# Optimization experiments

Hardware: AMD Instinct MI355X
Metric: run time of the kernel (lower is better)

## Reference

```python
import jax, jax.numpy as jnp
import numpy as np

EMBED = 512
HEADS = 8
DIM_HEAD = 64
SCALE = DIM_HEAD ** -0.5


def setup_inputs() -> dict:
    key = jax.random.key(0)
    k1, k2, k3 = jax.random.split(key, 3)
    x = jax.random.normal(k1, (1, EMBED, 64, 64), dtype=jnp.float32)
    # nn.Linear(embed, 3*embed) weight [out, in] -> store transposed [in, out] for x @ W
    W_qkv = jax.random.normal(k2, (EMBED, 3 * EMBED), dtype=jnp.float32) * (EMBED ** -0.5)
    b_qkv = jax.random.normal(k3, (3 * EMBED,), dtype=jnp.float32) * 0.01
    return {"x": x, "W_qkv": W_qkv, "b_qkv": b_qkv}


def reference(x, W_qkv, b_qkv):
    B, E, h, w = x.shape
    N = h * w
    # [B, E, H, W] -> [B, N, E]
    xs = x.reshape(B, E, N).transpose(0, 2, 1)
    qkv = xs @ W_qkv + b_qkv                      # [B, N, 3E]
    q, k, v = jnp.split(qkv, 3, axis=-1)          # each [B, N, E]

    def heads(t):
        return t.reshape(B, N, HEADS, DIM_HEAD).transpose(0, 2, 1, 3)  # [B, H, N, dh]

    q, k, v = heads(q), heads(k), heads(v)
    # raw (non-softmax) attention scores, materialized as in the original
    attn = jnp.einsum('bhqd,bhkd->bhqk', q, k) * SCALE  # [B, H, N, N]
    coarse_attn = attn.sum(axis=-2)                     # sum over queries -> [B, H, N]
    output = jnp.einsum('bhqk,bhkd->bhqd', attn, v)     # [B, H, N, dh]
    return coarse_attn, output
```

## Files before the change

### kernel.cpp

```cpp
#include <hip/hip_runtime.h>


#define N_TOK 4096
#define EMBED 512
#define J3    1536
#define HEADS 8
#define DH    64
#define SCALE 0.125f

typedef float  floatx4  __attribute__((ext_vector_type(4)));
typedef short  shortx8  __attribute__((ext_vector_type(8)));
typedef unsigned short ushortx4 __attribute__((ext_vector_type(4)));
typedef unsigned int u32;
typedef unsigned short ushort;

__device__ inline ushort f2bf(float f) {
    union { float f; u32 u; } x; x.f = f;
    u32 r = x.u + 0x7fffu + ((x.u >> 16) & 1u);
    return (ushort)(r >> 16);
}
__device__ inline float bf2f(ushort u) {
    union { u32 u; float f; } x; x.u = ((u32)u) << 16; return x.f;
}
__device__ static inline void async_copy16(void* lds, const void* g) {
    auto* gp = (const __attribute__((address_space(1))) u32*)g;
    auto* lp = (__attribute__((address_space(3))) u32*)lds;
    __builtin_amdgcn_global_load_lds(gp, lp, 16, 0, 0);
}
__device__ inline int permj(int j) {
    if (j < 512) return j;
    if (j < 1024) return 512 + ((j - 512) >> 6) * 128 + ((j - 512) & 63);
    return 512 + ((j - 1024) >> 6) * 128 + 64 + ((j - 1024) & 63);
}

__global__ __launch_bounds__(256) void prep(const float* __restrict__ x,
                                            const float* __restrict__ W,
                                            ushort* __restrict__ xT,
                                            ushort* __restrict__ WT,
                                            float* __restrict__ xsum) {
    const int t = threadIdx.x;
    int bx = blockIdx.x;
    const bool isx = bx < 64;
    const float* src = isx ? x : W;
    const int C = isx ? N_TOK : J3;
    if (!isx) bx -= 64;
    __shared__ float T[64][65];
    __shared__ float red[256];
    const int c0 = bx * 64, r0 = blockIdx.y * 64;
    #pragma unroll
    for (int k = 0; k < 16; ++k) {
        int i = t + 256 * k; int r = i >> 6, c = i & 63;
        T[r][c] = src[(size_t)(r0 + r) * C + c0 + c];
    }
    __syncthreads();
    if (isx) {
        int row = t >> 2, seg = (t & 3) * 16;
        float s = 0.f;
        #pragma unroll
        for (int cc = 0; cc < 16; ++cc) s += T[row][seg + cc];
        red[t] = s;
    }
    #pragma unroll
    for (int k = 0; k < 4; ++k) {
        int i = t + 256 * k; int cr = i >> 4, cc4 = (i & 15) * 4;
        ushortx4 o = { f2bf(T[cc4 + 0][cr]), f2bf(T[cc4 + 1][cr]),
                       f2bf(T[cc4 + 2][cr]), f2bf(T[cc4 + 3][cr]) };
        int dr = isx ? (c0 + cr) : permj(c0 + cr);
        ushort* dst = isx ? xT : WT;
        *(ushortx4*)&dst[(size_t)dr * 512 + r0 + cc4] = o;
    }
    if (isx) {
        __syncthreads();
        if ((t & 3) == 0)
            atomicAdd(&xsum[r0 + (t >> 2)], red[t] + red[t + 1] + red[t + 2] + red[t + 3]);
    }
}

__global__ __launch_bounds__(256) void qkv_m(const ushort* __restrict__ xT,
                                             const ushort* __restrict__ WT,
                                             const float* __restrict__ bias,
                                             ushort* __restrict__ qkv,
                                             float* __restrict__ Mp) {
    const int bx = blockIdx.x, ch = blockIdx.y;
    const int j0 = bx * 128, n0 = ch * 128;
    const bool iskv = bx >= 4;
    const int h = bx - 4;
    __shared__ __align__(16) char lds[34816];
    short* As = (short*)lds;
    short* Bs = (short*)(lds + 8192);
    short* Kt = (short*)lds;
    short* Vt = (short*)(lds + 17408);
    const int t = threadIdx.x, lane = t & 63, w = t >> 6;
    const int wm = w & 1, wn = w >> 1;
    const int quad = lane >> 4, mrow = lane & 15;
    floatx4 acc[4][4] = {};
    for (int e0 = 0; e0 < 512; e0 += 32) {
        __syncthreads();
        #pragma unroll
        for (int s = 0; s < 2; ++s) {
            int i = t + 256 * s; int row = i >> 2, q = i & 3;
            async_copy16((char*)As + (size_t)w * 1024 + (size_t)s * 4096,
                         xT + (size_t)(n0 + row) * 512 + e0 + q * 8);
            async_copy16((char*)Bs + (size_t)w * 1024 + (size_t)s * 4096,
                         WT + (size_t)(j0 + row) * 512 + e0 + q * 8);
        }
        __syncthreads();
        shortx8 a[4], b[4];
        #pragma unroll
        for (int mi = 0; mi < 4; ++mi)
            a[mi] = *(const shortx8*)&As[(wm * 64 + mi * 16 + mrow) * 32 + quad * 8];
        #pragma unroll
        for (int ni = 0; ni < 4; ++ni)
            b[ni] = *(const shortx8*)&Bs[(wn * 64 + ni * 16 + mrow) * 32 + quad * 8];
        #pragma unroll
        for (int mi = 0; mi < 4; ++mi)
            #pragma unroll
            for (int ni = 0; ni < 4; ++ni)
                acc[mi][ni] = __builtin_amdgcn_mfma_f32_16x16x32_bf16(a[mi], b[ni], acc[mi][ni], 0, 0, 0);
    }
    __syncthreads();
    {
        short* ldst = (wn == 0) ? Kt : Vt;
        #pragma unroll
        for (int ni = 0; ni < 4; ++ni) {
            int cl = wn * 64 + ni * 16 + mrow;
            float bj;
            if (!iskv) bj = bias[j0 + cl];
            else bj = (cl < 64) ? bias[512 + h * 64 + cl] : bias[1024 + h * 64 + cl - 64];
            int dh = ni * 16 + mrow;
            #pragma unroll
            for (int mi = 0; mi < 4; ++mi)
                #pragma unroll
                for (int r = 0; r < 4; ++r) {
                    int tok = wm * 64 + mi * 16 + quad * 4 + r;
                    float v = acc[mi][ni][r] + bj;
                    ushort bf = f2bf(v);
                    if (!iskv) {
                        qkv[(size_t)(n0 + tok) * J3 + j0 + cl] = bf;
                    } else {
                        ldst[dh * 136 + tok] = (short)bf;
                        if (cl < 64)
                            qkv[(size_t)(n0 + tok) * J3 + 512 + h * 128 + cl] = bf;
                    }
                }
        }
    }
    if (!iskv) return;
    __syncthreads();
    const int dpb = (w & 1) * 32, db = (w >> 1) * 32;
    floatx4 m[2][2] = {};
    #pragma unroll
    for (int kt = 0; kt < 4; ++kt) {
        shortx8 ka[2], vb[2];
        #pragma unroll
        for (int fi = 0; fi < 2; ++fi)
            ka[fi] = *(const shortx8*)&Kt[(dpb + fi * 16 + mrow) * 136 + kt * 32 + quad * 8];
        #pragma unroll
        for (int fj = 0; fj < 2; ++fj)
            vb[fj] = *(const shortx8*)&Vt[(db + fj * 16 + mrow) * 136 + kt * 32 + quad * 8];
        #pragma unroll
        for (int fi = 0; fi < 2; ++fi)
            #pragma unroll
            for (int fj = 0; fj < 2; ++fj)
                m[fi][fj] = __builtin_amdgcn_mfma_f32_16x16x32_bf16(ka[fi], vb[fj], m[fi][fj], 0, 0, 0);
    }
    float* mp = Mp + ((size_t)h * 32 + ch) * 4096;
    #pragma unroll
    for (int fi = 0; fi < 2; ++fi)
        #pragma unroll
        for (int fj = 0; fj < 2; ++fj)
            #pragma unroll
            for (int r = 0; r < 4; ++r)
                mp[(dpb + fi * 16 + quad * 4 + r) * 64 + db + fj * 16 + mrow] = m[fi][fj][r];
}

__global__ __launch_bounds__(256) void reduce_qm(const float* __restrict__ Mp,
                                                 const ushort* __restrict__ WT,
                                                 const float* __restrict__ bias,
                                                 const float* __restrict__ xsum,
                                                 ushort* __restrict__ Mt,
                                                 float* __restrict__ qsum) {
    const int h = blockIdx.x, part = blockIdx.y;
    const int t = threadIdx.x;
    __shared__ float Msh[16][68];
    __shared__ float red[256];
    const int i0 = part * 1024 + t * 4;
    floatx4 s = {0.f, 0.f, 0.f, 0.f};
    #pragma unroll 4
    for (int c = 0; c < 32; ++c)
        s += *(const floatx4*)&Mp[((size_t)h * 32 + c) * 4096 + i0];
    const int dpl = t >> 4, d0 = (t & 15) * 4;
    *(floatx4*)&Msh[dpl][d0] = s;
    __syncthreads();
    {
        int d = t >> 2, dpl0 = (t & 3) * 4;
        ushortx4 o = { f2bf(Msh[dpl0 + 0][d]), f2bf(Msh[dpl0 + 1][d]),
                       f2bf(Msh[dpl0 + 2][d]), f2bf(Msh[dpl0 + 3][d]) };
        *(ushortx4*)&Mt[(size_t)h * 4096 + d * 64 + part * 16 + dpl0] = o;
    }
    {
        int row = t >> 4, seg = (t & 15) * 32;
        int j = h * 64 + part * 16 + row;
        float qa = 0.f;
        #pragma unroll
        for (int g = 0; g < 4; ++g) {
            shortx8 wv = *(const shortx8*)(WT + (size_t)j * 512 + seg + g * 8);
            #pragma unroll
            for (int u = 0; u < 8; ++u)
                qa += bf2f((ushort)wv[u]) * xsum[seg + g * 8 + u];
        }
        red[t] = qa;
    }
    __syncthreads();
    if (t < 16) {
        float tot = 0.f;
        #pragma unroll
        for (int g = 0; g < 16; ++g) tot += red[t * 16 + g];
        int j = h * 64 + part * 16 + t;
        qsum[j] = 4096.f * bias[j] + tot;
    }
}

__global__ __launch_bounds__(64) void out_kernel(const ushort* __restrict__ qkv,
                                                 const ushort* __restrict__ Mt,
                                                 const float* __restrict__ qsum,
                                                 float* __restrict__ out) {
    const int h = blockIdx.x, n0 = blockIdx.y * 64;
    const int lane = threadIdx.x;
    const int quad = lane >> 4, mrow = lane & 15;
    floatx4 acc[4][4] = {};
    #pragma unroll
    for (int ks = 0; ks < 2; ++ks) {
        shortx8 a[4], b[4];
        #pragma unroll
        for (int mi = 0; mi < 4; ++mi)
            a[mi] = *(const shortx8*)(qkv + (size_t)(n0 + mi * 16 + mrow) * J3 + h * DH + ks * 32 + quad * 8);
        #pragma unroll
        for (int ni = 0; ni < 4; ++ni)
            b[ni] = *(const shortx8*)(Mt + (size_t)h * 4096 + (ni * 16 + mrow) * 64 + ks * 32 + quad * 8);
        #pragma unroll
        for (int mi = 0; mi < 4; ++mi)
            #pragma unroll
            for (int ni = 0; ni < 4; ++ni)
                acc[mi][ni] = __builtin_amdgcn_mfma_f32_16x16x32_bf16(a[mi], b[ni], acc[mi][ni], 0, 0, 0);
    }
    float* op = out + HEADS * N_TOK + (size_t)h * N_TOK * DH;
    #pragma unroll
    for (int mi = 0; mi < 4; ++mi)
        #pragma unroll
        for (int r = 0; r < 4; ++r) {
            int n = n0 + mi * 16 + quad * 4 + r;
            #pragma unroll
            for (int ni = 0; ni < 4; ++ni)
                op[(size_t)n * DH + ni * 16 + mrow] = acc[mi][ni][r] * SCALE;
        }
    float ca = 0.f;
    #pragma unroll
    for (int g = 0; g < 8; ++g) {
        shortx8 kk = *(const shortx8*)(qkv + (size_t)(n0 + lane) * J3 + 512 + h * 128 + g * 8);
        #pragma unroll
        for (int j = 0; j < 8; ++j)
            ca += bf2f((ushort)kk[j]) * qsum[h * DH + g * 8 + j];
    }
    out[h * N_TOK + n0 + lane] = ca * SCALE;
}

extern "C" void kernel_launch(void* const* d_in, const int* in_sizes, int n_in,
                              void* d_out, int out_size, void* d_ws, size_t ws_size,
                              hipStream_t stream) {
    const float* x = (const float*)d_in[0];
    const float* W = (const float*)d_in[1];
    const float* b = (const float*)d_in[2];
    float* out = (float*)d_out;

    ushort* xT = (ushort*)d_ws;
    ushort* WT = xT + (size_t)N_TOK * EMBED;
    ushort* qkvb = WT + (size_t)J3 * EMBED;
    ushort* Mt = qkvb + (size_t)N_TOK * J3;
    float* Mp   = (float*)(Mt + (size_t)HEADS * DH * DH);
    float* xsum = Mp + (size_t)HEADS * 32 * 4096;
    float* qsum = xsum + 512;

    prep<<<dim3(88, 8), 256, 0, stream>>>(x, W, xT, WT, xsum);
    qkv_m<<<dim3(12, 32), 256, 0, stream>>>(xT, WT, b, qkvb, Mp);
    reduce_qm<<<dim3(8, 4), 256, 0, stream>>>(Mp, WT, b, xsum, Mt, qsum);
    out_kernel<<<dim3(8, 64), 64, 0, stream>>>(qkvb, Mt, qsum, out);
}
```

Baseline: 99.91 us.

## Fuse QKV GEMM, M reduction and output into one persistent kernel with grid barriers

```diff
diff --git a/kernel.cpp b/kernel.cpp
--- a/kernel.cpp
+++ b/kernel.cpp
@@ -31,6 +31,14 @@
     if (j < 512) return j;
     if (j < 1024) return 512 + ((j - 512) >> 6) * 128 + ((j - 512) & 63);
     return 512 + ((j - 1024) >> 6) * 128 + 64 + ((j - 1024) & 63);
+}
+__device__ inline void bar_add(int* p) {
+    __hip_atomic_fetch_add(p, 1, __ATOMIC_ACQ_REL, __HIP_MEMORY_SCOPE_AGENT);
+}
+__device__ inline void bar_spin(int* p, int tgt) {
+    while (__hip_atomic_load(p, __ATOMIC_RELAXED, __HIP_MEMORY_SCOPE_AGENT) < tgt)
+        __builtin_amdgcn_s_sleep(8);
+    (void)__hip_atomic_load(p, __ATOMIC_ACQUIRE, __HIP_MEMORY_SCOPE_AGENT);
 }
 
 __global__ __launch_bounds__(256) void prep(const float* __restrict__ x,
@@ -76,11 +84,15 @@
     }
 }
 
-__global__ __launch_bounds__(256) void qkv_m(const ushort* __restrict__ xT,
-                                             const ushort* __restrict__ WT,
-                                             const float* __restrict__ bias,
-                                             ushort* __restrict__ qkv,
-                                             float* __restrict__ Mp) {
+__global__ __launch_bounds__(256, 2) void mega(const ushort* __restrict__ xT,
+                                               const ushort* __restrict__ WT,
+                                               const float* __restrict__ bias,
+                                               const float* __restrict__ xsum,
+                                               ushort* __restrict__ Mt,
+                                               float* __restrict__ Mp,
+                                               float* __restrict__ qsum,
+                                               int* __restrict__ bars,
+                                               float* __restrict__ out) {
     const int bx = blockIdx.x, ch = blockIdx.y;
     const int j0 = bx * 128, n0 = ch * 128;
     const bool iskv = bx >= 4;
@@ -90,9 +102,13 @@
     short* Bs = (short*)(lds + 8192);
     short* Kt = (short*)lds;
     short* Vt = (short*)(lds + 17408);
+    short* Qt = (short*)lds;
+    __shared__ float Msh[16][68];
+    __shared__ float red[256];
     const int t = threadIdx.x, lane = t & 63, w = t >> 6;
     const int wm = w & 1, wn = w >> 1;
     const int quad = lane >> 4, mrow = lane & 15;
+
     floatx4 acc[4][4] = {};
     for (int e0 = 0; e0 < 512; e0 += 32) {
         __syncthreads();
@@ -119,150 +135,151 @@
                 acc[mi][ni] = __builtin_amdgcn_mfma_f32_16x16x32_bf16(a[mi], b[ni], acc[mi][ni], 0, 0, 0);
     }
     __syncthreads();
-    {
-        short* ldst = (wn == 0) ? Kt : Vt;
+
+    if (!iskv) {
         #pragma unroll
         for (int ni = 0; ni < 4; ++ni) {
             int cl = wn * 64 + ni * 16 + mrow;
-            float bj;
-            if (!iskv) bj = bias[j0 + cl];
-            else bj = (cl < 64) ? bias[512 + h * 64 + cl] : bias[1024 + h * 64 + cl - 64];
-            int dh = ni * 16 + mrow;
+            float bj = bias[j0 + cl];
             #pragma unroll
             for (int mi = 0; mi < 4; ++mi)
                 #pragma unroll
                 for (int r = 0; r < 4; ++r) {
                     int tok = wm * 64 + mi * 16 + quad * 4 + r;
-                    float v = acc[mi][ni][r] + bj;
-                    ushort bf = f2bf(v);
-                    if (!iskv) {
-                        qkv[(size_t)(n0 + tok) * J3 + j0 + cl] = bf;
-                    } else {
-                        ldst[dh * 136 + tok] = (short)bf;
-                        if (cl < 64)
-                            qkv[(size_t)(n0 + tok) * J3 + 512 + h * 128 + cl] = bf;
-                    }
+                    Qt[tok * 136 + cl] = (short)f2bf(acc[mi][ni][r] + bj);
                 }
         }
-    }
-    if (!iskv) return;
+    } else {
+        short* ldst = (wn == 0) ? Kt : Vt;
+        const int boff = (wn == 0) ? 512 : 1024;
+        #pragma unroll
+        for (int ni = 0; ni < 4; ++ni) {
+            int dh = ni * 16 + mrow;
+            float bj = bias[boff + h * 64 + dh];
+            #pragma unroll
+            for (int mi = 0; mi < 4; ++mi)
+                #pragma unroll
+                for (int r = 0; r < 4; ++r) {
+                    int tok = wm * 64 + mi * 16 + quad * 4 + r;
+                    ldst[dh * 136 + tok] = (short)f2bf(acc[mi][ni][r] + bj);
+                }
+        }
+    }
     __syncthreads();
-    const int dpb = (w & 1) * 32, db = (w >> 1) * 32;
-    floatx4 m[2][2] = {};
-    #pragma unroll
-    for (int kt = 0; kt < 4; ++kt) {
-        shortx8 ka[2], vb[2];
+
+    if (iskv) {
+        const int dpb = (w & 1) * 32, db = (w >> 1) * 32;
+        floatx4 m[2][2] = {};
+        #pragma unroll
+        for (int kt = 0; kt < 4; ++kt) {
+            shortx8 ka[2], vb[2];
+            #pragma unroll
+            for (int fi = 0; fi < 2; ++fi)
+                ka[fi] = *(const shortx8*)&Kt[(dpb + fi * 16 + mrow) * 136 + kt * 32 + quad * 8];
+            #pragma unroll
+            for (int fj = 0; fj < 2; ++fj)
+                vb[fj] = *(const shortx8*)&Vt[(db + fj * 16 + mrow) * 136 + kt * 32 + quad * 8];
+            #pragma unroll
+            for (int fi = 0; fi < 2; ++fi)
+                #pragma unroll
+                for (int fj = 0; fj < 2; ++fj)
+                    m[fi][fj] = __builtin_amdgcn_mfma_f32_16x16x32_bf16(ka[fi], vb[fj], m[fi][fj], 0, 0, 0);
+        }
+        float* mp = Mp + ((size_t)h * 32 + ch) * 4096;
         #pragma unroll
         for (int fi = 0; fi < 2; ++fi)
-            ka[fi] = *(const shortx8*)&Kt[(dpb + fi * 16 + mrow) * 136 + kt * 32 + quad * 8];
-        #pragma unroll
-        for (int fj = 0; fj < 2; ++fj)
-            vb[fj] = *(const shortx8*)&Vt[(db + fj * 16 + mrow) * 136 + kt * 32 + quad * 8];
-        #pragma unroll
-        for (int fi = 0; fi < 2; ++fi)
             #pragma unroll
             for (int fj = 0; fj < 2; ++fj)
-                m[fi][fj] = __builtin_amdgcn_mfma_f32_16x16x32_bf16(ka[fi], vb[fj], m[fi][fj], 0, 0, 0);
-    }
-    float* mp = Mp + ((size_t)h * 32 + ch) * 4096;
-    #pragma unroll
-    for (int fi = 0; fi < 2; ++fi)
-        #pragma unroll
-        for (int fj = 0; fj < 2; ++fj)
-            #pragma unroll
-            for (int r = 0; r < 4; ++r)
-                mp[(dpb + fi * 16 + quad * 4 + r) * 64 + db + fj * 16 + mrow] = m[fi][fj][r];
-}
-
-__global__ __launch_bounds__(256) void reduce_qm(const float* __restrict__ Mp,
-                                                 const ushort* __restrict__ WT,
-                                                 const float* __restrict__ bias,
-                                                 const float* __restrict__ xsum,
-                                                 ushort* __restrict__ Mt,
-                                                 float* __restrict__ qsum) {
-    const int h = blockIdx.x, part = blockIdx.y;
-    const int t = threadIdx.x;
-    __shared__ float Msh[16][68];
-    __shared__ float red[256];
-    const int i0 = part * 1024 + t * 4;
-    floatx4 s = {0.f, 0.f, 0.f, 0.f};
-    #pragma unroll 4
-    for (int c = 0; c < 32; ++c)
-        s += *(const floatx4*)&Mp[((size_t)h * 32 + c) * 4096 + i0];
-    const int dpl = t >> 4, d0 = (t & 15) * 4;
-    *(floatx4*)&Msh[dpl][d0] = s;
-    __syncthreads();
-    {
-        int d = t >> 2, dpl0 = (t & 3) * 4;
-        ushortx4 o = { f2bf(Msh[dpl0 + 0][d]), f2bf(Msh[dpl0 + 1][d]),
-                       f2bf(Msh[dpl0 + 2][d]), f2bf(Msh[dpl0 + 3][d]) };
-        *(ushortx4*)&Mt[(size_t)h * 4096 + d * 64 + part * 16 + dpl0] = o;
-    }
-    {
-        int row = t >> 4, seg = (t & 15) * 32;
-        int j = h * 64 + part * 16 + row;
-        float qa = 0.f;
-        #pragma unroll
-        for (int g = 0; g < 4; ++g) {
-            shortx8 wv = *(const shortx8*)(WT + (size_t)j * 512 + seg + g * 8);
-            #pragma unroll
-            for (int u = 0; u < 8; ++u)
-                qa += bf2f((ushort)wv[u]) * xsum[seg + g * 8 + u];
-        }
-        red[t] = qa;
-    }
-    __syncthreads();
-    if (t < 16) {
-        float tot = 0.f;
-        #pragma unroll
-        for (int g = 0; g < 16; ++g) tot += red[t * 16 + g];
-        int j = h * 64 + part * 16 + t;
-        qsum[j] = 4096.f * bias[j] + tot;
-    }
-}
-
-__global__ __launch_bounds__(64) void out_kernel(const ushort* __restrict__ qkv,
-                                                 const ushort* __restrict__ Mt,
-                                                 const float* __restrict__ qsum,
-                                                 float* __restrict__ out) {
-    const int h = blockIdx.x, n0 = blockIdx.y * 64;
-    const int lane = threadIdx.x;
-    const int quad = lane >> 4, mrow = lane & 15;
-    floatx4 acc[4][4] = {};
-    #pragma unroll
-    for (int ks = 0; ks < 2; ++ks) {
-        shortx8 a[4], b[4];
+                #pragma unroll
+                for (int r = 0; r < 4; ++r)
+                    mp[(dpb + fi * 16 + quad * 4 + r) * 64 + db + fj * 16 + mrow] = m[fi][fj][r];
+        __syncthreads();
+        if (t == 0) bar_add(&bars[0]);
+
+        if (ch < 4) {
+            if (t == 0) bar_spin(&bars[0], 256);
+            __syncthreads();
+            const int part = ch;
+            const int i0 = part * 1024 + t * 4;
+            floatx4 s = {0.f, 0.f, 0.f, 0.f};
+            #pragma unroll 4
+            for (int c = 0; c < 32; ++c)
+                s += *(const floatx4*)&Mp[((size_t)h * 32 + c) * 4096 + i0];
+            *(floatx4*)&Msh[t >> 4][(t & 15) * 4] = s;
+            {
+                int row = t >> 4, seg = (t & 15) * 32;
+                int j = h * 64 + part * 16 + row;
+                float qa = 0.f;
+                #pragma unroll
+                for (int g = 0; g < 4; ++g) {
+                    shortx8 wv = *(const shortx8*)(WT + (size_t)j * 512 + seg + g * 8);
+                    #pragma unroll
+                    for (int u = 0; u < 8; ++u)
+                        qa += bf2f((ushort)wv[u]) * xsum[seg + g * 8 + u];
+                }
+                red[t] = qa;
+            }
+            __syncthreads();
+            {
+                int d = t >> 2, dpl0 = (t & 3) * 4;
+                ushortx4 o = { f2bf(Msh[dpl0 + 0][d]), f2bf(Msh[dpl0 + 1][d]),
+                               f2bf(Msh[dpl0 + 2][d]), f2bf(Msh[dpl0 + 3][d]) };
+                *(ushortx4*)&Mt[(size_t)h * 4096 + d * 64 + part * 16 + dpl0] = o;
+            }
+            if (t < 16) {
+                float tot = 0.f;
+                #pragma unroll
+                for (int g = 0; g < 16; ++g) tot += red[t * 16 + g];
+                int j = h * 64 + part * 16 + t;
+                qsum[j] = 4096.f * bias[j] + tot;
+            }
+            __syncthreads();
+            if (t == 0) bar_add(&bars[1]);
+        }
+        if (t == 0) bar_spin(&bars[1], 32);
+        __syncthreads();
+        {
+            int tok = t >> 1, half = (t & 1) * 32;
+            float ca = 0.f;
+            #pragma unroll 8
+            for (int dp = half; dp < half + 32; ++dp)
+                ca += bf2f((ushort)Kt[dp * 136 + tok]) * qsum[h * 64 + dp];
+            red[t] = ca;
+        }
+        __syncthreads();
+        if (t < 128)
+            out[h * N_TOK + n0 + t] = (red[2 * t] + red[2 * t + 1]) * SCALE;
+    } else {
+        if (t == 0) bar_spin(&bars[1], 32);
+        __syncthreads();
+        const int h2 = 2 * bx + wn;
+        floatx4 a2[4][4] = {};
+        #pragma unroll
+        for (int ks = 0; ks < 2; ++ks) {
+            shortx8 a[4], b[4];
+            #pragma unroll
+            for (int mi = 0; mi < 4; ++mi)
+                a[mi] = *(const shortx8*)&Qt[(wm * 64 + mi * 16 + mrow) * 136 + wn * 64 + ks * 32 + quad * 8];
+            #pragma unroll
+            for (int ni = 0; ni < 4; ++ni)
+                b[ni] = *(const shortx8*)(Mt + (size_t)h2 * 4096 + (ni * 16 + mrow) * 64 + ks * 32 + quad * 8);
+            #pragma unroll
+            for (int mi = 0; mi < 4; ++mi)
+                #pragma unroll
+                for (int ni = 0; ni < 4; ++ni)
+                    a2[mi][ni] = __builtin_amdgcn_mfma_f32_16x16x32_bf16(a[mi], b[ni], a2[mi][ni], 0, 0, 0);
+        }
+        float* op = out + HEADS * N_TOK + (size_t)h2 * N_TOK * DH;
         #pragma unroll
         for (int mi = 0; mi < 4; ++mi)
-            a[mi] = *(const shortx8*)(qkv + (size_t)(n0 + mi * 16 + mrow) * J3 + h * DH + ks * 32 + quad * 8);
-        #pragma unroll
-        for (int ni = 0; ni < 4; ++ni)
-            b[ni] = *(const shortx8*)(Mt + (size_t)h * 4096 + (ni * 16 + mrow) * 64 + ks * 32 + quad * 8);
-        #pragma unroll
-        for (int mi = 0; mi < 4; ++mi)
-            #pragma unroll
-            for (int ni = 0; ni < 4; ++ni)
-                acc[mi][ni] = __builtin_amdgcn_mfma_f32_16x16x32_bf16(a[mi], b[ni], acc[mi][ni], 0, 0, 0);
-    }
-    float* op = out + HEADS * N_TOK + (size_t)h * N_TOK * DH;
-    #pragma unroll
-    for (int mi = 0; mi < 4; ++mi)
-        #pragma unroll
-        for (int r = 0; r < 4; ++r) {
-            int n = n0 + mi * 16 + quad * 4 + r;
-            #pragma unroll
-            for (int ni = 0; ni < 4; ++ni)
-                op[(size_t)n * DH + ni * 16 + mrow] = acc[mi][ni][r] * SCALE;
-        }
-    float ca = 0.f;
-    #pragma unroll
-    for (int g = 0; g < 8; ++g) {
-        shortx8 kk = *(const shortx8*)(qkv + (size_t)(n0 + lane) * J3 + 512 + h * 128 + g * 8);
-        #pragma unroll
-        for (int j = 0; j < 8; ++j)
-            ca += bf2f((ushort)kk[j]) * qsum[h * DH + g * 8 + j];
-    }
-    out[h * N_TOK + n0 + lane] = ca * SCALE;
+            #pragma unroll
+            for (int r = 0; r < 4; ++r) {
+                int n = n0 + wm * 64 + mi * 16 + quad * 4 + r;
+                #pragma unroll
+                for (int ni = 0; ni < 4; ++ni)
+                    op[(size_t)n * DH + ni * 16 + mrow] = a2[mi][ni][r] * SCALE;
+            }
+    }
 }
 
 extern "C" void kernel_launch(void* const* d_in, const int* in_sizes, int n_in,
@@ -275,14 +292,13 @@
 
     ushort* xT = (ushort*)d_ws;
     ushort* WT = xT + (size_t)N_TOK * EMBED;
-    ushort* qkvb = WT + (size_t)J3 * EMBED;
-    ushort* Mt = qkvb + (size_t)N_TOK * J3;
+    ushort* Mt = WT + (size_t)J3 * EMBED;
     float* Mp   = (float*)(Mt + (size_t)HEADS * DH * DH);
     float* xsum = Mp + (size_t)HEADS * 32 * 4096;
     float* qsum = xsum + 512;
-
+    int*   bars = (int*)(qsum + 512);
+
+    hipMemsetAsync(bars, 0, 2 * sizeof(int), stream);
     prep<<<dim3(88, 8), 256, 0, stream>>>(x, W, xT, WT, xsum);
-    qkv_m<<<dim3(12, 32), 256, 0, stream>>>(xT, WT, b, qkvb, Mp);
-    reduce_qm<<<dim3(8, 4), 256, 0, stream>>>(Mp, WT, b, xsum, Mt, qsum);
-    out_kernel<<<dim3(8, 64), 64, 0, stream>>>(qkvb, Mt, qsum, out);
-}
+    mega<<<dim3(12, 32), 256, 0, stream>>>(xT, WT, b, xsum, Mt, Mp, qsum, bars, out);
+}
```

Measured after the change: 123.4 us. 23.6% more time.

## Fuse coarse-attention into QKV kernel, halve token tile, drop K copy to global

Applied to the files above, without the earlier changes.

```diff
diff --git a/kernel.cpp b/kernel.cpp
--- a/kernel.cpp
+++ b/kernel.cpp
@@ -79,92 +79,143 @@
 __global__ __launch_bounds__(256) void qkv_m(const ushort* __restrict__ xT,
                                              const ushort* __restrict__ WT,
                                              const float* __restrict__ bias,
-                                             ushort* __restrict__ qkv,
-                                             float* __restrict__ Mp) {
+                                             const float* __restrict__ xsum,
+                                             ushort* __restrict__ Qb,
+                                             float* __restrict__ Mp,
+                                             float* __restrict__ out) {
     const int bx = blockIdx.x, ch = blockIdx.y;
-    const int j0 = bx * 128, n0 = ch * 128;
+    const int j0 = bx * 128, n0 = ch * 64;
     const bool iskv = bx >= 4;
     const int h = bx - 4;
-    __shared__ __align__(16) char lds[34816];
+    __shared__ __align__(16) char lds[18432];
     short* As = (short*)lds;
-    short* Bs = (short*)(lds + 8192);
+    short* Bs = (short*)(lds + 4096);
     short* Kt = (short*)lds;
-    short* Vt = (short*)(lds + 17408);
+    short* Vt = (short*)(lds + 9216);
+    short* Qt = (short*)lds;
+    __shared__ float cred[64 * 33];
+    __shared__ float qs[64];
     const int t = threadIdx.x, lane = t & 63, w = t >> 6;
-    const int wm = w & 1, wn = w >> 1;
     const int quad = lane >> 4, mrow = lane & 15;
-    floatx4 acc[4][4] = {};
+
+    if (iskv) {
+        int jl = t >> 2, seg = (t & 3) * 128;
+        const ushort* wr = WT + (size_t)(h * 64 + jl) * 512 + seg;
+        float qa = 0.f;
+        #pragma unroll
+        for (int g = 0; g < 16; ++g) {
+            shortx8 wv = *(const shortx8*)(wr + g * 8);
+            #pragma unroll
+            for (int u = 0; u < 8; ++u)
+                qa += bf2f((ushort)wv[u]) * xsum[seg + g * 8 + u];
+        }
+        cred[t] = qa;
+        __syncthreads();
+        if (t < 64)
+            qs[t] = 4096.f * bias[h * 64 + t]
+                  + cred[4 * t] + cred[4 * t + 1] + cred[4 * t + 2] + cred[4 * t + 3];
+    }
+
+    floatx4 acc[4][2] = {};
     for (int e0 = 0; e0 < 512; e0 += 32) {
         __syncthreads();
+        {
+            int row = t >> 2, q = t & 3;
+            async_copy16((char*)As + (size_t)w * 1024,
+                         xT + (size_t)(n0 + row) * 512 + e0 + q * 8);
+        }
         #pragma unroll
         for (int s = 0; s < 2; ++s) {
             int i = t + 256 * s; int row = i >> 2, q = i & 3;
-            async_copy16((char*)As + (size_t)w * 1024 + (size_t)s * 4096,
-                         xT + (size_t)(n0 + row) * 512 + e0 + q * 8);
             async_copy16((char*)Bs + (size_t)w * 1024 + (size_t)s * 4096,
                          WT + (size_t)(j0 + row) * 512 + e0 + q * 8);
         }
         __syncthreads();
-        shortx8 a[4], b[4];
+        shortx8 a[4], b[2];
         #pragma unroll
         for (int mi = 0; mi < 4; ++mi)
-            a[mi] = *(const shortx8*)&As[(wm * 64 + mi * 16 + mrow) * 32 + quad * 8];
-        #pragma unroll
-        for (int ni = 0; ni < 4; ++ni)
-            b[ni] = *(const shortx8*)&Bs[(wn * 64 + ni * 16 + mrow) * 32 + quad * 8];
+            a[mi] = *(const shortx8*)&As[(mi * 16 + mrow) * 32 + quad * 8];
+        #pragma unroll
+        for (int ni = 0; ni < 2; ++ni)
+            b[ni] = *(const shortx8*)&Bs[(w * 32 + ni * 16 + mrow) * 32 + quad * 8];
         #pragma unroll
         for (int mi = 0; mi < 4; ++mi)
             #pragma unroll
-            for (int ni = 0; ni < 4; ++ni)
+            for (int ni = 0; ni < 2; ++ni)
                 acc[mi][ni] = __builtin_amdgcn_mfma_f32_16x16x32_bf16(a[mi], b[ni], acc[mi][ni], 0, 0, 0);
     }
     __syncthreads();
-    {
-        short* ldst = (wn == 0) ? Kt : Vt;
-        #pragma unroll
-        for (int ni = 0; ni < 4; ++ni) {
-            int cl = wn * 64 + ni * 16 + mrow;
-            float bj;
-            if (!iskv) bj = bias[j0 + cl];
-            else bj = (cl < 64) ? bias[512 + h * 64 + cl] : bias[1024 + h * 64 + cl - 64];
-            int dh = ni * 16 + mrow;
+
+    if (!iskv) {
+        #pragma unroll
+        for (int ni = 0; ni < 2; ++ni) {
+            int cl = w * 32 + ni * 16 + mrow;
+            float bj = bias[j0 + cl];
             #pragma unroll
             for (int mi = 0; mi < 4; ++mi)
                 #pragma unroll
                 for (int r = 0; r < 4; ++r) {
-                    int tok = wm * 64 + mi * 16 + quad * 4 + r;
+                    int tok = mi * 16 + quad * 4 + r;
+                    Qt[tok * 136 + cl] = (short)f2bf(acc[mi][ni][r] + bj);
+                }
+        }
+        __syncthreads();
+        #pragma unroll
+        for (int k = 0; k < 4; ++k) {
+            int u = t + 256 * k; int row = u >> 4, seg = u & 15;
+            *(shortx8*)(Qb + (size_t)(n0 + row) * 512 + j0 + seg * 8) =
+                *(const shortx8*)&Qt[row * 136 + seg * 8];
+        }
+        return;
+    }
+
+    {
+        short* dst = (w < 2) ? Kt : Vt;
+        const int dhb = (w & 1) * 32;
+        const int boff = (w < 2) ? 512 : 1024;
+        float cp[16] = {};
+        #pragma unroll
+        for (int ni = 0; ni < 2; ++ni) {
+            int dh = dhb + ni * 16 + mrow;
+            float bj = bias[boff + h * 64 + dh];
+            float qv = qs[dh];
+            #pragma unroll
+            for (int mi = 0; mi < 4; ++mi)
+                #pragma unroll
+                for (int r = 0; r < 4; ++r) {
+                    int tok = mi * 16 + quad * 4 + r;
                     float v = acc[mi][ni][r] + bj;
-                    ushort bf = f2bf(v);
-                    if (!iskv) {
-                        qkv[(size_t)(n0 + tok) * J3 + j0 + cl] = bf;
-                    } else {
-                        ldst[dh * 136 + tok] = (short)bf;
-                        if (cl < 64)
-                            qkv[(size_t)(n0 + tok) * J3 + 512 + h * 128 + cl] = bf;
-                    }
+                    dst[dh * 72 + tok] = (short)f2bf(v);
+                    if (w < 2) cp[mi * 4 + r] += v * qv;
                 }
         }
-    }
-    if (!iskv) return;
+        if (w < 2) {
+            #pragma unroll
+            for (int mi = 0; mi < 4; ++mi)
+                #pragma unroll
+                for (int r = 0; r < 4; ++r)
+                    cred[(mi * 16 + quad * 4 + r) * 33 + w * 16 + mrow] = cp[mi * 4 + r];
+        }
+    }
     __syncthreads();
     const int dpb = (w & 1) * 32, db = (w >> 1) * 32;
     floatx4 m[2][2] = {};
     #pragma unroll
-    for (int kt = 0; kt < 4; ++kt) {
+    for (int kt = 0; kt < 2; ++kt) {
         shortx8 ka[2], vb[2];
         #pragma unroll
         for (int fi = 0; fi < 2; ++fi)
-            ka[fi] = *(const shortx8*)&Kt[(dpb + fi * 16 + mrow) * 136 + kt * 32 + quad * 8];
+            ka[fi] = *(const shortx8*)&Kt[(dpb + fi * 16 + mrow) * 72 + kt * 32 + quad * 8];
         #pragma unroll
         for (int fj = 0; fj < 2; ++fj)
-            vb[fj] = *(const shortx8*)&Vt[(db + fj * 16 + mrow) * 136 + kt * 32 + quad * 8];
+            vb[fj] = *(const shortx8*)&Vt[(db + fj * 16 + mrow) * 72 + kt * 32 + quad * 8];
         #pragma unroll
         for (int fi = 0; fi < 2; ++fi)
             #pragma unroll
             for (int fj = 0; fj < 2; ++fj)
                 m[fi][fj] = __builtin_amdgcn_mfma_f32_16x16x32_bf16(ka[fi], vb[fj], m[fi][fj], 0, 0, 0);
     }
-    float* mp = Mp + ((size_t)h * 32 + ch) * 4096;
+    float* mp = Mp + ((size_t)h * 64 + ch) * 4096;
     #pragma unroll
     for (int fi = 0; fi < 2; ++fi)
         #pragma unroll
@@ -172,97 +223,59 @@
             #pragma unroll
             for (int r = 0; r < 4; ++r)
                 mp[(dpb + fi * 16 + quad * 4 + r) * 64 + db + fj * 16 + mrow] = m[fi][fj][r];
-}
-
-__global__ __launch_bounds__(256) void reduce_qm(const float* __restrict__ Mp,
-                                                 const ushort* __restrict__ WT,
-                                                 const float* __restrict__ bias,
-                                                 const float* __restrict__ xsum,
-                                                 ushort* __restrict__ Mt,
-                                                 float* __restrict__ qsum) {
+    if (t < 64) {
+        float s = 0.f;
+        #pragma unroll
+        for (int c = 0; c < 32; ++c) s += cred[t * 33 + c];
+        out[h * N_TOK + n0 + t] = s * SCALE;
+    }
+}
+
+__global__ __launch_bounds__(256) void reduce_m(const float* __restrict__ Mp,
+                                                ushort* __restrict__ Mt) {
     const int h = blockIdx.x, part = blockIdx.y;
     const int t = threadIdx.x;
-    __shared__ float Msh[16][68];
-    __shared__ float red[256];
-    const int i0 = part * 1024 + t * 4;
-    floatx4 s = {0.f, 0.f, 0.f, 0.f};
-    #pragma unroll 4
-    for (int c = 0; c < 32; ++c)
-        s += *(const floatx4*)&Mp[((size_t)h * 32 + c) * 4096 + i0];
-    const int dpl = t >> 4, d0 = (t & 15) * 4;
-    *(floatx4*)&Msh[dpl][d0] = s;
-    __syncthreads();
-    {
-        int d = t >> 2, dpl0 = (t & 3) * 4;
-        ushortx4 o = { f2bf(Msh[dpl0 + 0][d]), f2bf(Msh[dpl0 + 1][d]),
-                       f2bf(Msh[dpl0 + 2][d]), f2bf(Msh[dpl0 + 3][d]) };
-        *(ushortx4*)&Mt[(size_t)h * 4096 + d * 64 + part * 16 + dpl0] = o;
-    }
-    {
-        int row = t >> 4, seg = (t & 15) * 32;
-        int j = h * 64 + part * 16 + row;
-        float qa = 0.f;
-        #pragma unroll
-        for (int g = 0; g < 4; ++g) {
-            shortx8 wv = *(const shortx8*)(WT + (size_t)j * 512 + seg + g * 8);
-            #pragma unroll
-            for (int u = 0; u < 8; ++u)
-                qa += bf2f((ushort)wv[u]) * xsum[seg + g * 8 + u];
-        }
-        red[t] = qa;
-    }
-    __syncthreads();
-    if (t < 16) {
-        float tot = 0.f;
-        #pragma unroll
-        for (int g = 0; g < 16; ++g) tot += red[t * 16 + g];
-        int j = h * 64 + part * 16 + t;
-        qsum[j] = 4096.f * bias[j] + tot;
-    }
-}
-
-__global__ __launch_bounds__(64) void out_kernel(const ushort* __restrict__ qkv,
-                                                 const ushort* __restrict__ Mt,
-                                                 const float* __restrict__ qsum,
-                                                 float* __restrict__ out) {
+    __shared__ float sh[4][64];
+    float s = 0.f;
+    for (int c = 0; c < 64; ++c)
+        s += Mp[((size_t)h * 64 + c) * 4096 + part * 256 + t];
+    sh[t >> 6][t & 63] = s;
+    __syncthreads();
+    if (t < 64) {
+        ushortx4 o = { f2bf(sh[0][t]), f2bf(sh[1][t]), f2bf(sh[2][t]), f2bf(sh[3][t]) };
+        *(ushortx4*)&Mt[(size_t)h * 4096 + t * 64 + part * 4] = o;
+    }
+}
+
+__global__ __launch_bounds__(256) void out_kernel(const ushort* __restrict__ Qb,
+                                                  const ushort* __restrict__ Mt,
+                                                  float* __restrict__ out) {
     const int h = blockIdx.x, n0 = blockIdx.y * 64;
-    const int lane = threadIdx.x;
+    const int t = threadIdx.x, lane = t & 63, w = t >> 6;
     const int quad = lane >> 4, mrow = lane & 15;
-    floatx4 acc[4][4] = {};
+    __shared__ float Os[64 * 68];
+    floatx4 acc[4] = {};
     #pragma unroll
     for (int ks = 0; ks < 2; ++ks) {
-        shortx8 a[4], b[4];
-        #pragma unroll
-        for (int mi = 0; mi < 4; ++mi)
-            a[mi] = *(const shortx8*)(qkv + (size_t)(n0 + mi * 16 + mrow) * J3 + h * DH + ks * 32 + quad * 8);
-        #pragma unroll
-        for (int ni = 0; ni < 4; ++ni)
-            b[ni] = *(const shortx8*)(Mt + (size_t)h * 4096 + (ni * 16 + mrow) * 64 + ks * 32 + quad * 8);
-        #pragma unroll
-        for (int mi = 0; mi < 4; ++mi)
-            #pragma unroll
-            for (int ni = 0; ni < 4; ++ni)
-                acc[mi][ni] = __builtin_amdgcn_mfma_f32_16x16x32_bf16(a[mi], b[ni], acc[mi][ni], 0, 0, 0);
-    }
-    float* op = out + HEADS * N_TOK + (size_t)h * N_TOK * DH;
-    #pragma unroll
-    for (int mi = 0; mi < 4; ++mi)
-        #pragma unroll
-        for (int r = 0; r < 4; ++r) {
-            int n = n0 + mi * 16 + quad * 4 + r;
-            #pragma unroll
-            for (int ni = 0; ni < 4; ++ni)
-                op[(size_t)n * DH + ni * 16 + mrow] = acc[mi][ni][r] * SCALE;
-        }
-    float ca = 0.f;
-    #pragma unroll
-    for (int g = 0; g < 8; ++g) {
-        shortx8 kk = *(const shortx8*)(qkv + (size_t)(n0 + lane) * J3 + 512 + h * 128 + g * 8);
-        #pragma unroll
-        for (int j = 0; j < 8; ++j)
-            ca += bf2f((ushort)kk[j]) * qsum[h * DH + g * 8 + j];
-    }
-    out[h * N_TOK + n0 + lane] = ca * SCALE;
+        shortx8 a = *(const shortx8*)(Qb + (size_t)(n0 + w * 16 + mrow) * 512 + h * DH + ks * 32 + quad * 8);
+        #pragma unroll
+        for (int ni = 0; ni < 4; ++ni) {
+            shortx8 b = *(const shortx8*)(Mt + (size_t)h * 4096 + (ni * 16 + mrow) * 64 + ks * 32 + quad * 8);
+            acc[ni] = __builtin_amdgcn_mfma_f32_16x16x32_bf16(a, b, acc[ni], 0, 0, 0);
+        }
+    }
+    #pragma unroll
+    for (int ni = 0; ni < 4; ++ni)
+        #pragma unroll
+        for (int r = 0; r < 4; ++r)
+            Os[(w * 16 + quad * 4 + r) * 68 + ni * 16 + mrow] = acc[ni][r] * SCALE;
+    __syncthreads();
+    float* op = out + HEADS * N_TOK + (size_t)h * N_TOK * DH + (size_t)n0 * DH;
+    #pragma unroll
+    for (int k = 0; k < 4; ++k) {
+        int u = t + 256 * k; int row = u >> 4, seg = u & 15;
+        *(floatx4*)(op + row * 64 + seg * 4) = *(const floatx4*)&Os[row * 68 + seg * 4];
+    }
 }
 
 extern "C" void kernel_launch(void* const* d_in, const int* in_sizes, int n_in,
@@ -275,14 +288,13 @@
 
     ushort* xT = (ushort*)d_ws;
     ushort* WT = xT + (size_t)N_TOK * EMBED;
-    ushort* qkvb = WT + (size_t)J3 * EMBED;
-    ushort* Mt = qkvb + (size_t)N_TOK * J3;
+    ushort* Qb = WT + (size_t)J3 * EMBED;
+    ushort* Mt = Qb + (size_t)N_TOK * EMBED;
     float* Mp   = (float*)(Mt + (size_t)HEADS * DH * DH);
-    float* xsum = Mp + (size_t)HEADS * 32 * 4096;
-    float* qsum = xsum + 512;
+    float* xsum = Mp + (size_t)HEADS * 64 * 4096;
 
     prep<<<dim3(88, 8), 256, 0, stream>>>(x, W, xT, WT, xsum);
-    qkv_m<<<dim3(12, 32), 256, 0, stream>>>(xT, WT, b, qkvb, Mp);
-    reduce_qm<<<dim3(8, 4), 256, 0, stream>>>(Mp, WT, b, xsum, Mt, qsum);
-    out_kernel<<<dim3(8, 64), 64, 0, stream>>>(qkvb, Mt, qsum, out);
-}
+    qkv_m<<<dim3(12, 64), 256, 0, stream>>>(xT, WT, b, xsum, Qb, Mp, out);
+    reduce_m<<<dim3(8, 16), 256, 0, stream>>>(Mp, Mt);
+    out_kernel<<<dim3(8, 64), 256, 0, stream>>>(Qb, Mt, out);
+}
```

Measured after the change: 106.9 us. +7.0%, slower.
